# Performance work log

Measured on AMD Instinct MI355X. Metric: run time of the kernel, lower is better.

Reference implementation:

```python
import jax, jax.numpy as jnp
import numpy as np

NUM_CLUSTERS = 128
C = NUM_CLUSTERS + 1  # bincount minlength = number_clusters + 1
SOFTMAX_TEMP = 1.0


def setup_inputs() -> dict:
    key = jax.random.key(0)
    k1, k2, k3, k4 = jax.random.split(key, 4)
    B, N, D = 32, 4096, 64
    Bc = 4  # clusters batch dim; heads = B // Bc = 8
    return {
        "queries": jax.random.normal(k1, (B, N, D), dtype=jnp.float32),
        "keys": jax.random.normal(k2, (B, N, D), dtype=jnp.float32),
        "values": jax.random.normal(k3, (B, N, D), dtype=jnp.float32),
        "clusters": jax.random.randint(k4, (Bc, N), 0, C).astype(jnp.int64),
    }


def _segment_sum_batched(x, groups, num_segments):
    # x: [B, N, D], groups: [B, N] -> [B, num_segments, D]
    return jax.vmap(lambda xb, gb: jax.ops.segment_sum(xb, gb, num_segments=num_segments))(x, groups)


def reference(queries, keys, values, clusters):
    B, N, D = queries.shape
    Bc = clusters.shape[0]
    rep = B // Bc
    g = clusters.astype(jnp.int32)
    # per-cluster counts (bincount with minlength=C)
    counts = jax.vmap(lambda gb: jax.ops.segment_sum(jnp.ones((N,), jnp.float32), gb, num_segments=C))(g)
    # repeat assignments/counts across heads: torch .repeat(rep, 1) == tile on dim 0
    groups = jnp.tile(g, (rep, 1))          # [B, N]
    counts = jnp.tile(counts, (rep, 1))     # [B, C]
    w = jnp.where(counts > 0, 1.0 / counts, 0.0)  # 1/counts (guard empty clusters)

    Q_center = _segment_sum_batched(queries, groups, C) * w[..., None]  # [B, C, D]
    K_center = _segment_sum_batched(keys, groups, C) * w[..., None]
    V_center = _segment_sum_batched(values, groups, C) * w[..., None]

    QK = jnp.einsum('bqd,bkd->bqk', Q_center, K_center)  # [B, C, C]
    A = jax.nn.softmax(SOFTMAX_TEMP * QK, axis=-1)
    # weighted softmax: reweight by key-cluster counts, renormalize
    A = A * counts[:, None, :]
    A_full = A / A.sum(axis=-1, keepdims=True)

    V = jnp.einsum('bqk,bkd->bqd', A_full, V_center)  # [B, C, D]
    # Broadcast centers back to all cluster members (gather)
    out = jnp.take_along_axis(V, groups[..., None], axis=1)  # [B, N, D]
    return out, A_full[:, :, 0]
```

## Files before the change

### kernel.cpp

```cpp
#include <hip/hip_runtime.h>

#define B_ 32
#define N_ 4096
#define D_ 64
#define C_ 129
#define BC_ 4
#define CG_ 33

__global__ __launch_bounds__(256) void k_sort(const int* __restrict__ cl,
                                              float* __restrict__ counts,
                                              int* __restrict__ offsets,
                                              int* __restrict__ sidx) {
    __shared__ int cnt[C_];
    __shared__ int base[C_ + 1];
    __shared__ int cur[C_];
    int bc = blockIdx.x, tid = threadIdx.x;
    for (int i = tid; i < C_; i += 256) { cnt[i] = 0; cur[i] = 0; }
    __syncthreads();
    const int* g = cl + bc * N_;
    for (int n = tid; n < N_; n += 256) atomicAdd(&cnt[g[n]], 1);
    __syncthreads();
    if (tid == 0) {
        int acc = 0;
        for (int c = 0; c < C_; c++) { base[c] = acc; acc += cnt[c]; }
        base[C_] = acc;
    }
    __syncthreads();
    for (int i = tid; i < C_; i += 256) {
        counts[bc * C_ + i] = (float)cnt[i];
        offsets[bc * (C_ + 1) + i] = base[i];
    }
    if (tid == 0) offsets[bc * (C_ + 1) + C_] = N_;
    for (int n = tid; n < N_; n += 256) {
        int c = g[n];
        int pos = base[c] + atomicAdd(&cur[c], 1);
        sidx[bc * N_ + pos] = n;
    }
}

__global__ __launch_bounds__(256) void k_segsum2(const float* __restrict__ q,
                                                 const float* __restrict__ k,
                                                 const float* __restrict__ v,
                                                 const int* __restrict__ offsets,
                                                 const int* __restrict__ sidx,
                                                 float* __restrict__ sums) {
    int bid = blockIdx.x;
    int cg = bid % CG_;
    int t = (bid / CG_) % 3;
    int b = bid / (CG_ * 3);
    int wave = threadIdx.x >> 6, lane = threadIdx.x & 63;
    int c = cg * 4 + wave;
    if (c >= C_) return;
    int bc = b & 3;
    int start = offsets[bc * (C_ + 1) + c];
    int end = offsets[bc * (C_ + 1) + c + 1];
    const float* src = (t == 0) ? q : (t == 1) ? k : v;
    const float4* src4 = (const float4*)(src + (size_t)b * N_ * D_);
    const int* si = sidx + bc * N_;
    int sub = lane >> 4, d4 = lane & 15;
    float4 acc = make_float4(0.f, 0.f, 0.f, 0.f);
    for (int i = start + sub; i < end; i += 4) {
        int row = si[i];
        float4 val = src4[row * 16 + d4];
        acc.x += val.x; acc.y += val.y; acc.z += val.z; acc.w += val.w;
    }
    for (int off = 16; off <= 32; off <<= 1) {
        acc.x += __shfl_xor(acc.x, off, 64);
        acc.y += __shfl_xor(acc.y, off, 64);
        acc.z += __shfl_xor(acc.z, off, 64);
        acc.w += __shfl_xor(acc.w, off, 64);
    }
    int cnt = end - start;
    float w = (cnt > 0) ? 1.f / (float)cnt : 0.f;
    if (sub == 0) {
        float4 o = make_float4(acc.x * w, acc.y * w, acc.z * w, acc.w * w);
        ((float4*)(sums + ((size_t)t * B_ + b) * C_ * D_))[c * 16 + d4] = o;
    }
}

__global__ __launch_bounds__(256) void k_attn(const float* __restrict__ sums,
                                              const float* __restrict__ counts,
                                              float* __restrict__ vout,
                                              float* __restrict__ aout) {
    __shared__ float4 kc4[C_ * 17];
    __shared__ float4 vc4[C_ * 17];
    __shared__ float4 qr4[16 * 16];
    __shared__ float cnt_s[C_];
    __shared__ float arow[4][4][132];

    int b = blockIdx.x / 9;
    int qg = blockIdx.x % 9;
    int q0 = qg * 16;
    int qcnt = min(16, C_ - q0);
    int tid = threadIdx.x;

    for (int i = tid; i < C_; i += 256)
        cnt_s[i] = counts[(b & 3) * C_ + i];
    __syncthreads();

    const float4* qsum4 = (const float4*)(sums + (size_t)b * C_ * D_);
    const float4* ksum4 = (const float4*)(sums + ((size_t)B_ + b) * C_ * D_);
    const float4* vsum4 = (const float4*)(sums + ((size_t)2 * B_ + b) * C_ * D_);

    for (int i = tid; i < C_ * 16; i += 256) {
        int c = i >> 4, d4 = i & 15;
        kc4[c * 17 + d4] = ksum4[i];
        vc4[c * 17 + d4] = vsum4[i];
    }
    for (int i = tid; i < qcnt * 16; i += 256) {
        int r = i >> 4, d4 = i & 15;
        qr4[i] = qsum4[(q0 + r) * 16 + d4];
    }
    __syncthreads();

    int wave = tid >> 6, lane = tid & 63;

    for (int tt = wave; tt * 4 < qcnt; tt += 4) {
        int t4 = tt * 4;
        float s0[4] = {0, 0, 0, 0}, s1[4] = {0, 0, 0, 0}, s2[4] = {0, 0, 0, 0};
        for (int d4 = 0; d4 < 16; d4++) {
            float4 kv0 = kc4[lane * 17 + d4];
            float4 kv1 = kc4[(lane + 64) * 17 + d4];
            float4 kv2 = kc4[128 * 17 + d4];
#pragma unroll
            for (int r = 0; r < 4; r++) {
                int rr = t4 + r; if (rr >= qcnt) rr = qcnt - 1;
                float4 qv = qr4[rr * 16 + d4];
                s0[r] += qv.x * kv0.x + qv.y * kv0.y + qv.z * kv0.z + qv.w * kv0.w;
                s1[r] += qv.x * kv1.x + qv.y * kv1.y + qv.z * kv1.z + qv.w * kv1.w;
                s2[r] += qv.x * kv2.x + qv.y * kv2.y + qv.z * kv2.z + qv.w * kv2.w;
            }
        }
#pragma unroll
        for (int r = 0; r < 4; r++) {
            if (t4 + r >= qcnt) break;
            int qrow = q0 + t4 + r;
            float m = fmaxf(s0[r], s1[r]);
            if (lane == 0) m = fmaxf(m, s2[r]);
            for (int off = 32; off > 0; off >>= 1)
                m = fmaxf(m, __shfl_xor(m, off, 64));
            float e0 = __expf(s0[r] - m) * cnt_s[lane];
            float e1 = __expf(s1[r] - m) * cnt_s[lane + 64];
            float e2 = (lane == 0) ? __expf(s2[r] - m) * cnt_s[128] : 0.f;
            float sum = e0 + e1 + e2;
            for (int off = 32; off > 0; off >>= 1)
                sum += __shfl_xor(sum, off, 64);
            float inv = 1.f / sum;
            float a0 = e0 * inv, a1 = e1 * inv;
            arow[wave][r][lane] = a0;
            arow[wave][r][64 + lane] = a1;
            if (lane == 0) {
                arow[wave][r][128] = e2 * inv;
                aout[b * C_ + qrow] = a0;
            }
        }
        __builtin_amdgcn_s_waitcnt(0);
        int rr = lane >> 4, d4 = lane & 15;
        const float4* ar4 = (const float4*)arow[wave][rr];
        float4 o = make_float4(0.f, 0.f, 0.f, 0.f);
        for (int k4 = 0; k4 < 32; k4++) {
            float4 a4 = ar4[k4];
            float4 v0 = vc4[(k4 * 4 + 0) * 17 + d4];
            float4 v1 = vc4[(k4 * 4 + 1) * 17 + d4];
            float4 v2 = vc4[(k4 * 4 + 2) * 17 + d4];
            float4 v3 = vc4[(k4 * 4 + 3) * 17 + d4];
            o.x += a4.x * v0.x + a4.y * v1.x + a4.z * v2.x + a4.w * v3.x;
            o.y += a4.x * v0.y + a4.y * v1.y + a4.z * v2.y + a4.w * v3.y;
            o.z += a4.x * v0.z + a4.y * v1.z + a4.z * v2.z + a4.w * v3.z;
            o.w += a4.x * v0.w + a4.y * v1.w + a4.z * v2.w + a4.w * v3.w;
        }
        {
            float a128 = arow[wave][rr][128];
            float4 vv = vc4[128 * 17 + d4];
            o.x += a128 * vv.x; o.y += a128 * vv.y;
            o.z += a128 * vv.z; o.w += a128 * vv.w;
        }
        if (t4 + rr < qcnt) {
            float4* dst = (float4*)(vout + ((size_t)b * C_ + (q0 + t4 + rr)) * D_);
            dst[d4] = o;
        }
    }
}

__global__ __launch_bounds__(256) void k_gather(const float* __restrict__ vout,
                                                const int* __restrict__ cl,
                                                float* __restrict__ out) {
    int idx = blockIdx.x * 256 + threadIdx.x;
    int d4 = idx & 15;
    int n = (idx >> 4) & (N_ - 1);
    int b = idx >> 16;
    int c = cl[(b & 3) * N_ + n];
    const float4* src = (const float4*)(vout + ((size_t)b * C_ + c) * D_);
    ((float4*)out)[idx] = src[d4];
}

extern "C" void kernel_launch(void* const* d_in, const int* in_sizes, int n_in,
                              void* d_out, int out_size, void* d_ws, size_t ws_size,
                              hipStream_t stream) {
    const float* q = (const float*)d_in[0];
    const float* k = (const float*)d_in[1];
    const float* v = (const float*)d_in[2];
    const int* cl = (const int*)d_in[3];
    float* out = (float*)d_out;
    float* aout = out + (size_t)B_ * N_ * D_;

    float* ws = (float*)d_ws;
    float* counts = ws;
    float* sums = ws + 1024;
    float* vout = sums + (size_t)3 * B_ * C_ * D_;
    int* offsets = (int*)(vout + (size_t)B_ * C_ * D_);
    int* sidx = offsets + 4 * (C_ + 1);

    k_sort<<<BC_, 256, 0, stream>>>(cl, counts, offsets, sidx);
    k_segsum2<<<B_ * 3 * CG_, 256, 0, stream>>>(q, k, v, offsets, sidx, sums);
    k_attn<<<B_ * 9, 256, 0, stream>>>(sums, counts, vout, aout);
    k_gather<<<(B_ * N_ * 16) / 256, 256, 0, stream>>>(vout, cl, out);
}
```

Measured before the change: 175.2 us.

## Fuse Q/K/V segment sums per block with 4-way unrolled masked gathers; parallel prefix

The segment-sum kernel now handles queries, keys and values together in one block, so each sorted-index read serves three gathers. The loop is unrolled four-fold with clamped indices and float masks, which keeps twelve independent float4 loads in flight per iteration. The sort kernel's serial prefix sum is replaced by a per-thread O(C) partial sum. In exchange the grid has a third as many blocks and each thread holds more registers, which could lower occupancy.

```diff
diff --git a/kernel.cpp b/kernel.cpp
--- a/kernel.cpp
+++ b/kernel.cpp
@@ -12,7 +12,7 @@
                                               int* __restrict__ offsets,
                                               int* __restrict__ sidx) {
     __shared__ int cnt[C_];
-    __shared__ int base[C_ + 1];
+    __shared__ int base[C_];
     __shared__ int cur[C_];
     int bc = blockIdx.x, tid = threadIdx.x;
     for (int i = tid; i < C_; i += 256) { cnt[i] = 0; cur[i] = 0; }
@@ -20,10 +20,10 @@
     const int* g = cl + bc * N_;
     for (int n = tid; n < N_; n += 256) atomicAdd(&cnt[g[n]], 1);
     __syncthreads();
-    if (tid == 0) {
+    if (tid < C_) {
         int acc = 0;
-        for (int c = 0; c < C_; c++) { base[c] = acc; acc += cnt[c]; }
-        base[C_] = acc;
+        for (int i = 0; i < tid; i++) acc += cnt[i];
+        base[tid] = acc;
     }
     __syncthreads();
     for (int i = tid; i < C_; i += 256) {
@@ -38,7 +38,7 @@
     }
 }
 
-__global__ __launch_bounds__(256) void k_segsum2(const float* __restrict__ q,
+__global__ __launch_bounds__(256) void k_segsum3(const float* __restrict__ q,
                                                  const float* __restrict__ k,
                                                  const float* __restrict__ v,
                                                  const int* __restrict__ offsets,
@@ -46,35 +46,74 @@
                                                  float* __restrict__ sums) {
     int bid = blockIdx.x;
     int cg = bid % CG_;
-    int t = (bid / CG_) % 3;
-    int b = bid / (CG_ * 3);
+    int b = bid / CG_;
     int wave = threadIdx.x >> 6, lane = threadIdx.x & 63;
     int c = cg * 4 + wave;
     if (c >= C_) return;
     int bc = b & 3;
     int start = offsets[bc * (C_ + 1) + c];
     int end = offsets[bc * (C_ + 1) + c + 1];
-    const float* src = (t == 0) ? q : (t == 1) ? k : v;
-    const float4* src4 = (const float4*)(src + (size_t)b * N_ * D_);
+    int cnt = end - start;
+    int sub = lane >> 4, d4 = lane & 15;
+
+    const float4* q4 = (const float4*)(q + (size_t)b * N_ * D_);
+    const float4* k4 = (const float4*)(k + (size_t)b * N_ * D_);
+    const float4* v4 = (const float4*)(v + (size_t)b * N_ * D_);
     const int* si = sidx + bc * N_;
-    int sub = lane >> 4, d4 = lane & 15;
-    float4 acc = make_float4(0.f, 0.f, 0.f, 0.f);
-    for (int i = start + sub; i < end; i += 4) {
-        int row = si[i];
-        float4 val = src4[row * 16 + d4];
-        acc.x += val.x; acc.y += val.y; acc.z += val.z; acc.w += val.w;
-    }
+
+    float4 aq = make_float4(0.f, 0.f, 0.f, 0.f);
+    float4 ak = make_float4(0.f, 0.f, 0.f, 0.f);
+    float4 av = make_float4(0.f, 0.f, 0.f, 0.f);
+
+    if (cnt > 0) {
+        int last = end - 1;
+        for (int i0 = start; i0 < end; i0 += 16) {
+            int ia = i0 + sub, ib = ia + 4, ic = ia + 8, id = ia + 12;
+            int ra = si[min(ia, last)];
+            int rb = si[min(ib, last)];
+            int rc = si[min(ic, last)];
+            int rd = si[min(id, last)];
+            float ma = (ia < end) ? 1.f : 0.f;
+            float mb = (ib < end) ? 1.f : 0.f;
+            float mc = (ic < end) ? 1.f : 0.f;
+            float md = (id < end) ? 1.f : 0.f;
+            float4 qa = q4[ra * 16 + d4], qb = q4[rb * 16 + d4];
+            float4 qc = q4[rc * 16 + d4], qd = q4[rd * 16 + d4];
+            float4 ka = k4[ra * 16 + d4], kb = k4[rb * 16 + d4];
+            float4 kc = k4[rc * 16 + d4], kd = k4[rd * 16 + d4];
+            float4 va = v4[ra * 16 + d4], vb = v4[rb * 16 + d4];
+            float4 vc = v4[rc * 16 + d4], vd = v4[rd * 16 + d4];
+            aq.x += ma * qa.x + mb * qb.x + mc * qc.x + md * qd.x;
+            aq.y += ma * qa.y + mb * qb.y + mc * qc.y + md * qd.y;
+            aq.z += ma * qa.z + mb * qb.z + mc * qc.z + md * qd.z;
+            aq.w += ma * qa.w + mb * qb.w + mc * qc.w + md * qd.w;
+            ak.x += ma * ka.x + mb * kb.x + mc * kc.x + md * kd.x;
+            ak.y += ma * ka.y + mb * kb.y + mc * kc.y + md * kd.y;
+            ak.z += ma * ka.z + mb * kb.z + mc * kc.z + md * kd.z;
+            ak.w += ma * ka.w + mb * kb.w + mc * kc.w + md * kd.w;
+            av.x += ma * va.x + mb * vb.x + mc * vc.x + md * vd.x;
+            av.y += ma * va.y + mb * vb.y + mc * vc.y + md * vd.y;
+            av.z += ma * va.z + mb * vb.z + mc * vc.z + md * vd.z;
+            av.w += ma * va.w + mb * vb.w + mc * vc.w + md * vd.w;
+        }
+    }
+#pragma unroll
     for (int off = 16; off <= 32; off <<= 1) {
-        acc.x += __shfl_xor(acc.x, off, 64);
-        acc.y += __shfl_xor(acc.y, off, 64);
-        acc.z += __shfl_xor(acc.z, off, 64);
-        acc.w += __shfl_xor(acc.w, off, 64);
-    }
-    int cnt = end - start;
-    float w = (cnt > 0) ? 1.f / (float)cnt : 0.f;
+        aq.x += __shfl_xor(aq.x, off, 64); aq.y += __shfl_xor(aq.y, off, 64);
+        aq.z += __shfl_xor(aq.z, off, 64); aq.w += __shfl_xor(aq.w, off, 64);
+        ak.x += __shfl_xor(ak.x, off, 64); ak.y += __shfl_xor(ak.y, off, 64);
+        ak.z += __shfl_xor(ak.z, off, 64); ak.w += __shfl_xor(ak.w, off, 64);
+        av.x += __shfl_xor(av.x, off, 64); av.y += __shfl_xor(av.y, off, 64);
+        av.z += __shfl_xor(av.z, off, 64); av.w += __shfl_xor(av.w, off, 64);
+    }
     if (sub == 0) {
-        float4 o = make_float4(acc.x * w, acc.y * w, acc.z * w, acc.w * w);
-        ((float4*)(sums + ((size_t)t * B_ + b) * C_ * D_))[c * 16 + d4] = o;
+        float w = (cnt > 0) ? 1.f / (float)cnt : 0.f;
+        float4 oq = make_float4(aq.x * w, aq.y * w, aq.z * w, aq.w * w);
+        float4 ok = make_float4(ak.x * w, ak.y * w, ak.z * w, ak.w * w);
+        float4 ov = make_float4(av.x * w, av.y * w, av.z * w, av.w * w);
+        ((float4*)(sums + (size_t)b * C_ * D_))[c * 16 + d4] = oq;
+        ((float4*)(sums + ((size_t)B_ + b) * C_ * D_))[c * 16 + d4] = ok;
+        ((float4*)(sums + ((size_t)2 * B_ + b) * C_ * D_))[c * 16 + d4] = ov;
     }
 }
 
@@ -212,7 +251,7 @@
     int* sidx = offsets + 4 * (C_ + 1);
 
     k_sort<<<BC_, 256, 0, stream>>>(cl, counts, offsets, sidx);
-    k_segsum2<<<B_ * 3 * CG_, 256, 0, stream>>>(q, k, v, offsets, sidx, sums);
+    k_segsum3<<<B_ * CG_, 256, 0, stream>>>(q, k, v, offsets, sidx, sums);
     k_attn<<<B_ * 9, 256, 0, stream>>>(sums, counts, vout, aout);
     k_gather<<<(B_ * N_ * 16) / 256, 256, 0, stream>>>(vout, cl, out);
 }
```

Measured after the change: 172.4 us. Within noise of the previous version (-1.6%).
